# Kernel tuning notes

Measured on AMD Instinct MI355X. Metric: run time of the kernel, lower is better.

The kernel has to match this reference:

```python
import jax, jax.numpy as jnp
import numpy as np

TAU = 20.0
THRESHOLD = 1.0
RESET_V = 0.0
DT = 1.0
SIM_TIME = 100


def setup_inputs() -> dict:
    key = jax.random.key(0)
    ks = jax.random.split(key, 6)
    B, D, H, A = 8192, 256, 256, 64
    return {
        "x": jax.random.normal(ks[0], (B, D), dtype=jnp.float32),
        "enc_W": jax.random.normal(ks[1], (D, D), dtype=jnp.float32) * 0.1,  # Linear weight [out,in]
        "enc_b": jnp.zeros((D,), dtype=jnp.float32),
        "W1": jax.random.normal(ks[2], (D, H), dtype=jnp.float32) * 0.1,
        "W2": jax.random.normal(ks[3], (H, H), dtype=jnp.float32) * 0.1,
        "W3": jax.random.normal(ks[4], (H, A), dtype=jnp.float32) * 0.1,
    }


def _lif_step(v, inp, W, decay):
    # synaptic input -> leaky integrate -> fire -> reset
    syn = inp @ W
    v = v * decay + syn * (1.0 - decay)
    spikes = (v >= THRESHOLD).astype(v.dtype)
    v = jnp.where(spikes > 0, RESET_V, v)
    return v, spikes


def reference(x, enc_W, enc_b, W1, W2, W3):
    B = x.shape[0]
    decay = jnp.exp(jnp.asarray(-DT / TAU, dtype=x.dtype))
    # rate encoding: sigmoid(Linear(x)); constant input at every timestep
    rates = jax.nn.sigmoid(x @ enc_W.T + enc_b)

    H1, H2, A = W1.shape[1], W2.shape[1], W3.shape[1]
    init = (
        jnp.zeros((B, H1), x.dtype),
        jnp.zeros((B, H2), x.dtype),
        jnp.zeros((B, A), x.dtype),
        jnp.zeros((B, A), x.dtype),  # accumulated output spikes
    )

    def step(carry, _):
        v1, v2, v3, acc = carry
        v1, s1 = _lif_step(v1, rates, W1, decay)
        v2, s2 = _lif_step(v2, s1, W2, decay)
        v3, s3 = _lif_step(v3, s2, W3, decay)
        return (v1, v2, v3, acc + s3), None

    (_, _, _, acc), _ = jax.lax.scan(step, init, None, length=SIM_TIME)
    return acc / SIM_TIME
```

## Files before the change

### kernel.cpp

```cpp
#include <hip/hip_runtime.h>
#include <math.h>

#define SIM_T 100

__global__ __launch_bounds__(256) void k_transpose256(
    const float* __restrict__ W, float* __restrict__ WT) {
  int k = blockIdx.x;
  int o = threadIdx.x;
  WT[k * 256 + o] = W[o * 256 + k];
}

__global__ __launch_bounds__(256) void k_perm(const float* __restrict__ W2,
                                              float* __restrict__ W2p) {
  int i = blockIdx.x;
  int t = threadIdx.x;
  int l = t >> 2, q = t & 3;
  W2p[i * 256 + t] = W2[i * 256 + q * 64 + l];
}

template <int EPI>
__global__ __launch_bounds__(256, 2) void k_gemm64(
    const float* __restrict__ A,
    const float* __restrict__ WT,
    const float* __restrict__ bias,
    float* __restrict__ O,
    float omd) {
  __shared__ float4 sh4[64 * 64];
  float* shf = (float*)sh4;
  const int t = threadIdx.x;
  const int lane = t & 63;
  const int w = t >> 6;
  const int rt = blockIdx.x >> 2;
  const int cs = blockIdx.x & 3;
  const int colbase_v = cs * 64 + w * 16;
  const int colbase = __builtin_amdgcn_readfirstlane(colbase_v);

  {
    const float4* Ag = (const float4*)(A + (size_t)rt * 64 * 256);
#pragma unroll
    for (int i = 0; i < 16; i++) {
      int g = i * 256 + t;
      int row = g >> 6, kt = g & 63;
      sh4[row * 64 + (kt ^ row)] = Ag[g];
    }
  }
  __syncthreads();

  const float* wp = WT + colbase;
  float acc[16];
#pragma unroll
  for (int c = 0; c < 16; c++) acc[c] = 0.f;

  for (int kt = 0; kt < 64; kt++) {
    float4 xv = sh4[lane * 64 + (kt ^ lane)];
    const float* xf = &xv.x;
#pragma unroll
    for (int kk = 0; kk < 4; kk++) {
      const float* wk = wp + (kt * 4 + kk) * 256;
#pragma unroll
      for (int c = 0; c < 16; c++) acc[c] = fmaf(xf[kk], wk[c], acc[c]);
    }
  }
  __syncthreads();

  const int ccbase = (colbase_v & 63);
  if (EPI == 0) {
#pragma unroll
    for (int c = 0; c < 16; c++) {
      float v = acc[c] + bias[colbase + c];
      float r = 1.f / (1.f + expf(-v));
      int cc = ccbase + c;
      shf[lane * 64 + (cc ^ lane)] = r;
    }
  } else {
#pragma unroll
    for (int c = 0; c < 16; c++) {
      int cc = ccbase + c;
      shf[lane * 64 + (cc ^ lane)] = __fmul_rn(acc[c], omd);
    }
  }
  __syncthreads();

  float* Obase = O + (size_t)rt * 64 * 256 + cs * 64;
#pragma unroll
  for (int i = 0; i < 16; i++) {
    int g = i * 256 + t;
    int row = g >> 6, cc = g & 63;
    Obase[row * 256 + cc] = shf[row * 64 + (cc ^ row)];
  }
}

__global__ __launch_bounds__(256, 8) void k_sim(
    const float* __restrict__ c_in, const float* __restrict__ W2p,
    const float* __restrict__ W3, float* __restrict__ out, float decay,
    float omd) {
  const int lane = threadIdx.x & 63;
  const int row = blockIdx.x * 4 + (threadIdx.x >> 6);
  const float* crow = c_in + (long)row * 256;
  const float c0 = crow[lane];
  const float c1 = crow[64 + lane];
  const float c2 = crow[128 + lane];
  const float c3 = crow[192 + lane];
  float v10 = 0.f, v11 = 0.f, v12 = 0.f, v13 = 0.f;
  float v20 = 0.f, v21 = 0.f, v22 = 0.f, v23 = 0.f;
  float v3 = 0.f;
  int acc = 0;
  const float4* w2p = (const float4*)W2p + lane;

  for (int t = 0; t < SIM_T; t++) {
    v10 = __fadd_rn(__fmul_rn(v10, decay), c0);
    bool f0 = v10 >= 1.f;
    unsigned long long m0 = __ballot(f0);
    v10 = f0 ? 0.f : v10;
    v11 = __fadd_rn(__fmul_rn(v11, decay), c1);
    bool f1 = v11 >= 1.f;
    unsigned long long m1 = __ballot(f1);
    v11 = f1 ? 0.f : v11;
    v12 = __fadd_rn(__fmul_rn(v12, decay), c2);
    bool f2 = v12 >= 1.f;
    unsigned long long m2 = __ballot(f2);
    v12 = f2 ? 0.f : v12;
    v13 = __fadd_rn(__fmul_rn(v13, decay), c3);
    bool f3 = v13 >= 1.f;
    unsigned long long m3 = __ballot(f3);
    v13 = f3 ? 0.f : v13;

    float s0 = 0.f, s1 = 0.f, s2 = 0.f, s3 = 0.f;
#define ACC2(mask, qb)                            \
  {                                               \
    unsigned long long m = (mask);                \
    while (m) {                                   \
      int i = __builtin_ctzll(m) + (qb);          \
      m &= m - 1;                                 \
      float4 w = w2p[i * 64];                     \
      s0 += w.x;                                  \
      s1 += w.y;                                  \
      s2 += w.z;                                  \
      s3 += w.w;                                  \
    }                                             \
  }
    ACC2(m0, 0)
    ACC2(m1, 64)
    ACC2(m2, 128)
    ACC2(m3, 192)

    v20 = __fadd_rn(__fmul_rn(v20, decay), __fmul_rn(s0, omd));
    bool g0 = v20 >= 1.f;
    unsigned long long n0 = __ballot(g0);
    v20 = g0 ? 0.f : v20;
    v21 = __fadd_rn(__fmul_rn(v21, decay), __fmul_rn(s1, omd));
    bool g1 = v21 >= 1.f;
    unsigned long long n1 = __ballot(g1);
    v21 = g1 ? 0.f : v21;
    v22 = __fadd_rn(__fmul_rn(v22, decay), __fmul_rn(s2, omd));
    bool g2 = v22 >= 1.f;
    unsigned long long n2 = __ballot(g2);
    v22 = g2 ? 0.f : v22;
    v23 = __fadd_rn(__fmul_rn(v23, decay), __fmul_rn(s3, omd));
    bool g3 = v23 >= 1.f;
    unsigned long long n3 = __ballot(g3);
    v23 = g3 ? 0.f : v23;

    float z = 0.f;
    if (n0 | n1 | n2 | n3) {
#define ACC3(mask, qb)                            \
  {                                               \
    unsigned long long m = (mask);                \
    while (m) {                                   \
      int i = __builtin_ctzll(m) + (qb);          \
      m &= m - 1;                                 \
      z += W3[i * 64 + lane];                     \
    }                                             \
  }
      ACC3(n0, 0)
      ACC3(n1, 64)
      ACC3(n2, 128)
      ACC3(n3, 192)
    }
    v3 = __fadd_rn(__fmul_rn(v3, decay), __fmul_rn(z, omd));
    bool h = v3 >= 1.f;
    acc += h ? 1 : 0;
    v3 = h ? 0.f : v3;
  }
  out[(long)row * 64 + lane] = __fdiv_rn((float)acc, 100.f);
}

extern "C" void kernel_launch(void* const* d_in, const int* in_sizes, int n_in,
                              void* d_out, int out_size, void* d_ws,
                              size_t ws_size, hipStream_t stream) {
  const float* x = (const float*)d_in[0];
  const float* encW = (const float*)d_in[1];
  const float* encB = (const float*)d_in[2];
  const float* W1 = (const float*)d_in[3];
  const float* W2 = (const float*)d_in[4];
  const float* W3 = (const float*)d_in[5];
  float* out = (float*)d_out;

  float* c = (float*)d_ws;
  float* rates = (float*)d_ws + 2097152;
  float* W2p = (float*)d_ws + 4194304;
  float* encWT = (float*)d_ws + 4194304 + 65536;

  const float decay = (float)exp((double)(-0.05f));
  const float omd = 1.0f - decay;

  k_transpose256<<<256, 256, 0, stream>>>(encW, encWT);
  k_perm<<<256, 256, 0, stream>>>(W2, W2p);
  k_gemm64<0><<<512, 256, 0, stream>>>(x, encWT, encB, rates, omd);
  k_gemm64<1><<<512, 256, 0, stream>>>(rates, W1, encB, c, omd);
  k_sim<<<2048, 256, 0, stream>>>(c, W2p, W3, out, decay, omd);
}
```

Before: 189.7 us.

## Replace LDS-staged GEMM with register-streamed rows and narrower column tiles

The two dense GEMMs (encoder and W1) no longer stage the A tile through swizzled shared memory. Each thread now loads its own row directly into registers in four phases of 64 k-values, and each block computes 32 columns instead of 64, doubling the grid to 1024 blocks. Outputs are written straight to global memory as float4 instead of going through an LDS transpose. The change drops the LDS staging and barriers and raises occupancy. In exchange, each thread's row loads are strided across lanes and therefore uncoalesced, and A is read more times because there are more column groups.

```diff
diff --git a/kernel.cpp b/kernel.cpp
--- a/kernel.cpp
+++ b/kernel.cpp
@@ -19,74 +19,70 @@
 }
 
 template <int EPI>
-__global__ __launch_bounds__(256, 2) void k_gemm64(
+__global__ __launch_bounds__(256, 4) void k_gemm_rs(
     const float* __restrict__ A,
     const float* __restrict__ WT,
     const float* __restrict__ bias,
     float* __restrict__ O,
     float omd) {
-  __shared__ float4 sh4[64 * 64];
-  float* shf = (float*)sh4;
   const int t = threadIdx.x;
   const int lane = t & 63;
   const int w = t >> 6;
-  const int rt = blockIdx.x >> 2;
-  const int cs = blockIdx.x & 3;
-  const int colbase_v = cs * 64 + w * 16;
+  const int rt = blockIdx.x >> 3;
+  const int cg = blockIdx.x & 7;
+  const int row = rt * 64 + lane;
+  const int colbase_v = cg * 32 + w * 8;
   const int colbase = __builtin_amdgcn_readfirstlane(colbase_v);
-
-  {
-    const float4* Ag = (const float4*)(A + (size_t)rt * 64 * 256);
+  const float4* arow4 = (const float4*)(A + (size_t)row * 256);
+  const float* wp = WT + colbase;
+
+  float acc[8];
+#pragma unroll
+  for (int c = 0; c < 8; c++) acc[c] = 0.f;
+
+#pragma unroll
+  for (int ph = 0; ph < 4; ph++) {
+    float4 a[16];
+#pragma unroll
+    for (int i = 0; i < 16; i++) a[i] = arow4[ph * 16 + i];
 #pragma unroll
     for (int i = 0; i < 16; i++) {
-      int g = i * 256 + t;
-      int row = g >> 6, kt = g & 63;
-      sh4[row * 64 + (kt ^ row)] = Ag[g];
-    }
-  }
-  __syncthreads();
-
-  const float* wp = WT + colbase;
-  float acc[16];
-#pragma unroll
-  for (int c = 0; c < 16; c++) acc[c] = 0.f;
-
-  for (int kt = 0; kt < 64; kt++) {
-    float4 xv = sh4[lane * 64 + (kt ^ lane)];
-    const float* xf = &xv.x;
-#pragma unroll
-    for (int kk = 0; kk < 4; kk++) {
-      const float* wk = wp + (kt * 4 + kk) * 256;
-#pragma unroll
-      for (int c = 0; c < 16; c++) acc[c] = fmaf(xf[kk], wk[c], acc[c]);
-    }
-  }
-  __syncthreads();
-
-  const int ccbase = (colbase_v & 63);
+      const float* af = &a[i].x;
+#pragma unroll
+      for (int kk = 0; kk < 4; kk++) {
+        const int k = ph * 64 + i * 4 + kk;
+        const float* wk = wp + k * 256;
+#pragma unroll
+        for (int c = 0; c < 8; c++) acc[c] = fmaf(af[kk], wk[c], acc[c]);
+      }
+    }
+  }
+
+  float* obase = O + (size_t)row * 256 + colbase_v;
   if (EPI == 0) {
-#pragma unroll
-    for (int c = 0; c < 16; c++) {
+    float4 r0, r1;
+    float* rf0 = &r0.x;
+    float* rf1 = &r1.x;
+#pragma unroll
+    for (int c = 0; c < 4; c++) {
       float v = acc[c] + bias[colbase + c];
-      float r = 1.f / (1.f + expf(-v));
-      int cc = ccbase + c;
-      shf[lane * 64 + (cc ^ lane)] = r;
-    }
+      rf0[c] = 1.f / (1.f + expf(-v));
+      float v2 = acc[c + 4] + bias[colbase + c + 4];
+      rf1[c] = 1.f / (1.f + expf(-v2));
+    }
+    *(float4*)obase = r0;
+    *(float4*)(obase + 4) = r1;
   } else {
-#pragma unroll
-    for (int c = 0; c < 16; c++) {
-      int cc = ccbase + c;
-      shf[lane * 64 + (cc ^ lane)] = __fmul_rn(acc[c], omd);
-    }
-  }
-  __syncthreads();
-
-  float* Obase = O + (size_t)rt * 64 * 256 + cs * 64;
-#pragma unroll
-  for (int i = 0; i < 16; i++) {
-    int g = i * 256 + t;
-    int row = g >> 6, cc = g & 63;
-    Obase[row * 256 + cc] = shf[row * 64 + (cc ^ row)];
+    float4 r0, r1;
+    float* rf0 = &r0.x;
+    float* rf1 = &r1.x;
+#pragma unroll
+    for (int c = 0; c < 4; c++) {
+      rf0[c] = __fmul_rn(acc[c], omd);
+      rf1[c] = __fmul_rn(acc[c + 4], omd);
+    }
+    *(float4*)obase = r0;
+    *(float4*)(obase + 4) = r1;
   }
 }
 
@@ -206,7 +202,7 @@
 
   k_transpose256<<<256, 256, 0, stream>>>(encW, encWT);
   k_perm<<<256, 256, 0, stream>>>(W2, W2p);
-  k_gemm64<0><<<512, 256, 0, stream>>>(x, encWT, encB, rates, omd);
-  k_gemm64<1><<<512, 256, 0, stream>>>(rates, W1, encB, c, omd);
+  k_gemm_rs<0><<<1024, 256, 0, stream>>>(x, encWT, encB, rates, omd);
+  k_gemm_rs<1><<<1024, 256, 0, stream>>>(rates, W1, encB, c, omd);
   k_sim<<<2048, 256, 0, stream>>>(c, W2p, W3, out, decay, omd);
 }
```

Measured after the change: 205.2 us. 8.2% more time.

## Restructure dense GEMMs to stage weight chunks in LDS with row-tile blocks

Applied to the files above, without the earlier changes.

Each GEMM block now handles 16 rows across all 256 output columns. The weight matrix is streamed through shared memory in 32-row chunks, and activations are read as float4 broadcasts from LDS. Before, each wave fetched weights as scalar global loads and results were transposed back through a swizzled shared buffer. Output is now written directly as float4 rows, which removes the epilogue shuffle but means every block reloads the full weight matrix and adds barriers per chunk.

```diff
diff --git a/kernel.cpp b/kernel.cpp
--- a/kernel.cpp
+++ b/kernel.cpp
@@ -19,74 +19,93 @@
 }
 
 template <int EPI>
-__global__ __launch_bounds__(256, 2) void k_gemm64(
+__global__ __launch_bounds__(256, 3) void k_gemm_lds(
     const float* __restrict__ A,
     const float* __restrict__ WT,
     const float* __restrict__ bias,
     float* __restrict__ O,
     float omd) {
-  __shared__ float4 sh4[64 * 64];
-  float* shf = (float*)sh4;
+  __shared__ float4 lds_a[16 * 64];
+  __shared__ float4 lds_w[32 * 64];
   const int t = threadIdx.x;
   const int lane = t & 63;
   const int w = t >> 6;
-  const int rt = blockIdx.x >> 2;
-  const int cs = blockIdx.x & 3;
-  const int colbase_v = cs * 64 + w * 16;
-  const int colbase = __builtin_amdgcn_readfirstlane(colbase_v);
-
-  {
-    const float4* Ag = (const float4*)(A + (size_t)rt * 64 * 256);
-#pragma unroll
-    for (int i = 0; i < 16; i++) {
-      int g = i * 256 + t;
-      int row = g >> 6, kt = g & 63;
-      sh4[row * 64 + (kt ^ row)] = Ag[g];
-    }
-  }
+  const int rowbase = blockIdx.x * 16;
+
+  const float4* Ag = (const float4*)(A + (size_t)rowbase * 256);
+  const float4* Wg = (const float4*)WT;
+
+#pragma unroll
+  for (int i = 0; i < 4; i++) lds_a[i * 256 + t] = Ag[i * 256 + t];
+#pragma unroll
+  for (int i = 0; i < 8; i++) lds_w[i * 256 + t] = Wg[i * 256 + t];
   __syncthreads();
 
-  const float* wp = WT + colbase;
-  float acc[16];
-#pragma unroll
-  for (int c = 0; c < 16; c++) acc[c] = 0.f;
-
-  for (int kt = 0; kt < 64; kt++) {
-    float4 xv = sh4[lane * 64 + (kt ^ lane)];
-    const float* xf = &xv.x;
-#pragma unroll
-    for (int kk = 0; kk < 4; kk++) {
-      const float* wk = wp + (kt * 4 + kk) * 256;
-#pragma unroll
-      for (int c = 0; c < 16; c++) acc[c] = fmaf(xf[kk], wk[c], acc[c]);
-    }
-  }
-  __syncthreads();
-
-  const int ccbase = (colbase_v & 63);
+  float4 acc[4];
+#pragma unroll
+  for (int r = 0; r < 4; r++) acc[r] = make_float4(0.f, 0.f, 0.f, 0.f);
+
+  for (int kc = 0; kc < 8; kc++) {
+#pragma unroll
+    for (int kg = 0; kg < 8; kg++) {
+      float4 w0 = lds_w[(kg * 4 + 0) * 64 + lane];
+      float4 w1 = lds_w[(kg * 4 + 1) * 64 + lane];
+      float4 w2 = lds_w[(kg * 4 + 2) * 64 + lane];
+      float4 w3 = lds_w[(kg * 4 + 3) * 64 + lane];
+#pragma unroll
+      for (int r = 0; r < 4; r++) {
+        float4 a = lds_a[(w * 4 + r) * 64 + (kc * 8 + kg)];
+        acc[r].x = fmaf(a.x, w0.x, acc[r].x);
+        acc[r].y = fmaf(a.x, w0.y, acc[r].y);
+        acc[r].z = fmaf(a.x, w0.z, acc[r].z);
+        acc[r].w = fmaf(a.x, w0.w, acc[r].w);
+        acc[r].x = fmaf(a.y, w1.x, acc[r].x);
+        acc[r].y = fmaf(a.y, w1.y, acc[r].y);
+        acc[r].z = fmaf(a.y, w1.z, acc[r].z);
+        acc[r].w = fmaf(a.y, w1.w, acc[r].w);
+        acc[r].x = fmaf(a.z, w2.x, acc[r].x);
+        acc[r].y = fmaf(a.z, w2.y, acc[r].y);
+        acc[r].z = fmaf(a.z, w2.z, acc[r].z);
+        acc[r].w = fmaf(a.z, w2.w, acc[r].w);
+        acc[r].x = fmaf(a.w, w3.x, acc[r].x);
+        acc[r].y = fmaf(a.w, w3.y, acc[r].y);
+        acc[r].z = fmaf(a.w, w3.z, acc[r].z);
+        acc[r].w = fmaf(a.w, w3.w, acc[r].w);
+      }
+    }
+    if (kc < 7) {
+      __syncthreads();
+#pragma unroll
+      for (int i = 0; i < 8; i++)
+        lds_w[i * 256 + t] = Wg[(kc + 1) * 2048 + i * 256 + t];
+      __syncthreads();
+    }
+  }
+
+  float4* O4 = (float4*)O;
   if (EPI == 0) {
-#pragma unroll
-    for (int c = 0; c < 16; c++) {
-      float v = acc[c] + bias[colbase + c];
-      float r = 1.f / (1.f + expf(-v));
-      int cc = ccbase + c;
-      shf[lane * 64 + (cc ^ lane)] = r;
+    float4 b = ((const float4*)bias)[lane];
+#pragma unroll
+    for (int r = 0; r < 4; r++) {
+      int row = rowbase + w * 4 + r;
+      float4 o;
+      o.x = 1.f / (1.f + expf(-(acc[r].x + b.x)));
+      o.y = 1.f / (1.f + expf(-(acc[r].y + b.y)));
+      o.z = 1.f / (1.f + expf(-(acc[r].z + b.z)));
+      o.w = 1.f / (1.f + expf(-(acc[r].w + b.w)));
+      O4[(size_t)row * 64 + lane] = o;
     }
   } else {
 #pragma unroll
-    for (int c = 0; c < 16; c++) {
-      int cc = ccbase + c;
-      shf[lane * 64 + (cc ^ lane)] = __fmul_rn(acc[c], omd);
-    }
-  }
-  __syncthreads();
-
-  float* Obase = O + (size_t)rt * 64 * 256 + cs * 64;
-#pragma unroll
-  for (int i = 0; i < 16; i++) {
-    int g = i * 256 + t;
-    int row = g >> 6, cc = g & 63;
-    Obase[row * 256 + cc] = shf[row * 64 + (cc ^ row)];
+    for (int r = 0; r < 4; r++) {
+      int row = rowbase + w * 4 + r;
+      float4 o;
+      o.x = __fmul_rn(acc[r].x, omd);
+      o.y = __fmul_rn(acc[r].y, omd);
+      o.z = __fmul_rn(acc[r].z, omd);
+      o.w = __fmul_rn(acc[r].w, omd);
+      O4[(size_t)row * 64 + lane] = o;
+    }
   }
 }
 
@@ -206,7 +225,7 @@
 
   k_transpose256<<<256, 256, 0, stream>>>(encW, encWT);
   k_perm<<<256, 256, 0, stream>>>(W2, W2p);
-  k_gemm64<0><<<512, 256, 0, stream>>>(x, encWT, encB, rates, omd);
-  k_gemm64<1><<<512, 256, 0, stream>>>(rates, W1, encB, c, omd);
+  k_gemm_lds<0><<<512, 256, 0, stream>>>(x, encWT, encB, rates, omd);
+  k_gemm_lds<1><<<512, 256, 0, stream>>>(rates, W1, encB, c, omd);
   k_sim<<<2048, 256, 0, stream>>>(c, W2p, W3, out, decay, omd);
 }
```

After: 181.3 us. -4.4%, faster.
